# Performance work log

Measured on AMD Instinct MI355X. Metric: run time of the kernel, lower is better.

The kernel has to match this reference:

```python
import jax, jax.numpy as jnp
import numpy as np

N_NODES = 100000
N_EDGES = 1600000
DIM = 128
N_GRAPHS = 64
N_LAYERS = 7
LEAKY_SLOPE = 0.01
BN_EPS = 1e-5


def setup_inputs() -> dict:
    key = jax.random.key(0)
    ks = jax.random.split(key, 6)
    x = jax.random.normal(ks[0], (N_NODES, DIM), dtype=jnp.float32)
    edge_index = jax.random.randint(ks[1], (2, N_EDGES), 0, N_NODES, dtype=jnp.int64)
    batch = jnp.sort(jax.random.randint(ks[2], (N_NODES,), 0, N_GRAPHS, dtype=jnp.int64))
    # GCNConv weights (Glorot-ish scale), biases, BatchNorm affine params
    Ws = jax.random.normal(ks[3], (N_LAYERS, DIM, DIM), dtype=jnp.float32) * (1.0 / np.sqrt(DIM))
    bs = jnp.zeros((N_LAYERS, DIM), dtype=jnp.float32)
    gammas = jnp.ones((N_LAYERS, DIM), dtype=jnp.float32)
    betas = jnp.zeros((N_LAYERS, DIM), dtype=jnp.float32)
    return {"x": x, "edge_index": edge_index, "batch": batch,
            "Ws": Ws, "bs": bs, "gammas": gammas, "betas": betas}


def reference(x, edge_index, batch, Ws, bs, gammas, betas):
    N = x.shape[0]
    # Add self-loops once (shared by all 7 GCNConv layers)
    loops = jnp.arange(N, dtype=edge_index.dtype)
    src = jnp.concatenate([edge_index[0], loops])  # [E+N]
    dst = jnp.concatenate([edge_index[1], loops])  # [E+N]
    # Symmetric normalization: deg over destination (incl. self-loops)
    deg = jax.ops.segment_sum(jnp.ones_like(dst, dtype=x.dtype), dst, num_segments=N)
    dinv = jax.lax.rsqrt(jnp.maximum(deg, 1.0))  # deg >= 1 from self-loops
    norm = dinv[src] * dinv[dst]                 # [E+N]

    def block(h, W, b, gamma, beta):
        # GCNConv: linear -> gather -> normalized scatter-add
        h = h @ W + b                                            # [N, D]
        msgs = h[src] * norm[:, None]                            # [E+N, D]
        h = jax.ops.segment_sum(msgs, dst, num_segments=N)       # [N, D]
        # LeakyReLU then BatchNorm (batch statistics over nodes)
        h = jax.nn.leaky_relu(h, negative_slope=LEAKY_SLOPE)
        mu = jnp.mean(h, axis=0)
        var = jnp.mean((h - mu) ** 2, axis=0)
        h = (h - mu) * jax.lax.rsqrt(var + BN_EPS) * gamma + beta
        return h

    h = x
    for i in range(N_LAYERS):
        h = block(h, Ws[i], bs[i], gammas[i], betas[i])

    # global_mean_pool over graph ids
    sums = jax.ops.segment_sum(h, batch, num_segments=N_GRAPHS)          # [G, D]
    cnt = jax.ops.segment_sum(jnp.ones((N,), h.dtype), batch, num_segments=N_GRAPHS)
    return sums / jnp.maximum(cnt, 1.0)[:, None]
```

## Files before the change

### kernel.cpp

```cpp
#include <hip/hip_runtime.h>
#include <hip/hip_fp16.h>

#define DIMM 128
#define LEAKY_S 0.01f
#define EPS_BN 1e-5f

typedef _Float16 half8 __attribute__((ext_vector_type(8)));
typedef float f32x4 __attribute__((ext_vector_type(4)));


__global__ __launch_bounds__(256) void k_deg(const int* __restrict__ dst, int* __restrict__ deg, int E, int N) {
    int i = blockIdx.x * 256 + threadIdx.x;
    if (i < E) {
        int d = dst[i];
        if ((unsigned)d < (unsigned)N) atomicAdd(&deg[d], 1);
    }
}

__global__ __launch_bounds__(256) void k_dinv(const int* __restrict__ deg, float* __restrict__ dinv, int N) {
    int i = blockIdx.x * 256 + threadIdx.x;
    if (i < N) dinv[i] = rsqrtf((float)(deg[i] + 1));
}

__global__ __launch_bounds__(256) void k_scanA(const int* __restrict__ deg, int* __restrict__ bsum, int n) {
    __shared__ int ws[4];
    int tid = threadIdx.x, lane = tid & 63, wid = tid >> 6;
    int base = blockIdx.x * 1024;
    int s = 0;
    #pragma unroll
    for (int j = 0; j < 4; ++j) {
        int i = base + j * 256 + tid;
        if (i < n) s += deg[i];
    }
    #pragma unroll
    for (int off = 32; off > 0; off >>= 1) s += __shfl_down(s, (unsigned)off, 64);
    if (lane == 0) ws[wid] = s;
    __syncthreads();
    if (tid == 0) bsum[blockIdx.x] = ws[0] + ws[1] + ws[2] + ws[3];
}

__global__ __launch_bounds__(64) void k_scanB(const int* __restrict__ bsum, int* __restrict__ bofs,
                                              int* __restrict__ rowptr, int nb, int n) {
    if (threadIdx.x == 0) {
        int run = 0;
        for (int j = 0; j < nb; ++j) { bofs[j] = run; run += bsum[j]; }
        rowptr[n] = run;
    }
}

__global__ __launch_bounds__(1024) void k_scanC(const int* __restrict__ deg, const int* __restrict__ bofs,
                                                int* __restrict__ rowptr, int n) {
    __shared__ int wsum[16];
    int tid = threadIdx.x, lane = tid & 63, wid = tid >> 6;
    int i = blockIdx.x * 1024 + tid;
    int v = (i < n) ? deg[i] : 0;
    int s = v;
    #pragma unroll
    for (int off = 1; off < 64; off <<= 1) {
        int t = __shfl_up(s, (unsigned)off, 64);
        if (lane >= off) s += t;
    }
    if (lane == 63) wsum[wid] = s;
    __syncthreads();
    if (wid == 0 && lane < 16) {
        int ws = wsum[lane];
        #pragma unroll
        for (int off = 1; off < 16; off <<= 1) {
            int t = __shfl_up(ws, (unsigned)off, 64);
            if (lane >= off) ws += t;
        }
        wsum[lane] = ws;
    }
    __syncthreads();
    int woff = wid ? wsum[wid - 1] : 0;
    if (i < n) rowptr[i] = bofs[blockIdx.x] + woff + (s - v);
}

__global__ __launch_bounds__(256) void k_fill(const int* __restrict__ src, const int* __restrict__ dst,
                                              const int* __restrict__ rowptr, int* __restrict__ cursor,
                                              const float* __restrict__ dinv,
                                              int2* __restrict__ csr, int E, int N) {
    int i = blockIdx.x * 256 + threadIdx.x;
    if (i < E) {
        int d = dst[i], s = src[i];
        if ((unsigned)d < (unsigned)N && (unsigned)s < (unsigned)N) {
            int pos = atomicAdd(&cursor[d], 1);
            int idx = rowptr[d] + pos;
            csr[idx] = make_int2(s, __float_as_int(dinv[s] * dinv[d]));
        }
    }
}


__global__ __launch_bounds__(128) void k_wbn(const float* __restrict__ W, const float* __restrict__ bias,
                                             const float* __restrict__ stats, const float* __restrict__ gamma,
                                             const float* __restrict__ beta,
                                             __half* __restrict__ Wt, float* __restrict__ bias2,
                                             int ident, float inv_n) {
    __shared__ float red2[2];
    int n = blockIdx.x;
    int k = threadIdx.x;
    float a = 1.f, b = 0.f;
    if (!ident) {
        float mu  = stats[k] * inv_n;
        float var = stats[128 + k] * inv_n - mu * mu;
        a = gamma[k] * rsqrtf(var + EPS_BN);
        b = beta[k] - mu * a;
    }
    float w = W[k * DIMM + n];
    Wt[n * DIMM + k] = __float2half(a * w);
    float p = b * w;
    #pragma unroll
    for (int off = 32; off > 0; off >>= 1) p += __shfl_down(p, (unsigned)off, 64);
    if ((k & 63) == 0) red2[k >> 6] = p;
    __syncthreads();
    if (k == 0) bias2[n] = bias[n] + red2[0] + red2[1];
}


__global__ __launch_bounds__(256) void k_gemm(const void* __restrict__ A, const __half* __restrict__ Wt,
                                              const float* __restrict__ bias2,
                                              __half* __restrict__ out, int N, int a_half) {
    __shared__ char smem[128 * 256];
    int tid = threadIdx.x;
    int lane = tid & 63, wid = tid >> 6;
    int quad = lane >> 4, lm = lane & 15;
    int row0 = blockIdx.x * 128;

    const float*  Af = (const float*)A;
    const __half* Ah = (const __half*)A;
    #pragma unroll
    for (int it = 0; it < 8; ++it) {
        int i = it * 256 + tid;
        int r = i >> 4, c = i & 15;
        int gr = row0 + r;
        union { _Float16 h[8]; uint4 u; } pk;
        if (gr < N) {
            if (a_half) {
                pk.u = *(const uint4*)(Ah + (size_t)gr * DIMM + c * 8);
            } else {
                float4 f0 = *(const float4*)(Af + (size_t)gr * DIMM + c * 8);
                float4 f1 = *(const float4*)(Af + (size_t)gr * DIMM + c * 8 + 4);
                pk.h[0] = (_Float16)f0.x; pk.h[1] = (_Float16)f0.y;
                pk.h[2] = (_Float16)f0.z; pk.h[3] = (_Float16)f0.w;
                pk.h[4] = (_Float16)f1.x; pk.h[5] = (_Float16)f1.y;
                pk.h[6] = (_Float16)f1.z; pk.h[7] = (_Float16)f1.w;
            }
        } else {
            pk.u = make_uint4(0, 0, 0, 0);
        }
        *(uint4*)(smem + r * 256 + ((c ^ (r & 7)) << 4)) = pk.u;
    }

    f32x4 acc[2][8];
    #pragma unroll
    for (int c = 0; c < 8; ++c) {
        float bc = bias2[c * 16 + lm];
        acc[0][c] = (f32x4){bc, bc, bc, bc};
        acc[1][c] = acc[0][c];
    }
    __syncthreads();

    const _Float16* Wt16 = (const _Float16*)Wt;
    #pragma unroll
    for (int kc = 0; kc < 4; ++kc) {
        int sw = ((kc * 4 + quad) ^ (lm & 7)) << 4;
        half8 a0 = *(const half8*)(smem + (wid * 32 + lm) * 256 + sw);
        half8 a1 = *(const half8*)(smem + (wid * 32 + 16 + lm) * 256 + sw);
        #pragma unroll
        for (int c = 0; c < 8; ++c) {
            half8 b = *(const half8*)(Wt16 + (c * 16 + lm) * DIMM + kc * 32 + quad * 8);
            acc[0][c] = __builtin_amdgcn_mfma_f32_16x16x32_f16(a0, b, acc[0][c], 0, 0, 0);
            acc[1][c] = __builtin_amdgcn_mfma_f32_16x16x32_f16(a1, b, acc[1][c], 0, 0, 0);
        }
    }

    __syncthreads();
    #pragma unroll
    for (int r = 0; r < 2; ++r)
        #pragma unroll
        for (int c = 0; c < 8; ++c)
            #pragma unroll
            for (int i = 0; i < 4; ++i) {
                int rit = wid * 32 + r * 16 + quad * 4 + i;
                int col = c * 16 + lm;
                *(_Float16*)(smem + rit * 256 + col * 2) = (_Float16)acc[r][c][i];
            }
    __syncthreads();
    for (int i = tid; i < 128 * 16; i += 256) {
        int r = i >> 4, seg = i & 15;
        int gr = row0 + r;
        if (gr < N)
            ((uint4*)(out + (size_t)gr * DIMM))[seg] = ((const uint4*)(smem + r * 256))[seg];
    }
}


__global__ __launch_bounds__(256) void k_agg(const __half* __restrict__ t, __half* __restrict__ out,
                                             const int* __restrict__ rowptr, const int2* __restrict__ csr,
                                             const float* __restrict__ dinv,
                                             float* __restrict__ stats, int N, int nwaves) {
    int tid = threadIdx.x;
    int lane = tid & 63, wid = tid >> 6;
    int grp = lane >> 4;
    int l16 = lane & 15;
    int gw = blockIdx.x * 4 + wid;

    float sx[8] = {0.f, 0.f, 0.f, 0.f, 0.f, 0.f, 0.f, 0.f};
    float qx[8] = {0.f, 0.f, 0.f, 0.f, 0.f, 0.f, 0.f, 0.f};

    int node = gw;
    int e0 = 0, e1 = 0;
    float di = 0.f;
    int2 c[8];
    if (node < N) {
        e0 = rowptr[node]; e1 = rowptr[node + 1]; di = dinv[node];
        int last = e1 - 1;
        #pragma unroll
        for (int j = 0; j < 8; ++j) {
            int idx = e0 + 4 * j + grp;
            int idxc = idx < last ? idx : last;
            if (idxc < 0) idxc = 0;
            c[j] = csr[idxc];
            if (idx >= e1) c[j].y = 0;
        }
    }

    while (node < N) {
        int nxt = node + nwaves;
        int ep0 = 0, ep1 = 0;
        float dip = 0.f;
        if (nxt < N) { ep0 = rowptr[nxt]; ep1 = rowptr[nxt + 1]; dip = dinv[nxt]; }

        union { half8 h; __half2 h2[4]; } us;
        us.h = *(const half8*)(t + ((size_t)(unsigned)node << 7) + l16 * 8);

        float v[8] = {0.f, 0.f, 0.f, 0.f, 0.f, 0.f, 0.f, 0.f};

        #pragma unroll
        for (int j = 0; j < 8; ++j) {
            float wgt = __int_as_float(c[j].y);
            union { half8 h; __half2 h2[4]; } g;
            g.h = *(const half8*)(t + ((size_t)(unsigned)c[j].x << 7) + l16 * 8);
            #pragma unroll
            for (int p = 0; p < 4; ++p) {
                float2 f = __half22float2(g.h2[p]);
                v[2 * p]     = fmaf(wgt, f.x, v[2 * p]);
                v[2 * p + 1] = fmaf(wgt, f.y, v[2 * p + 1]);
            }
        }

        int2 cn[8];
        {
            int lastn = ep1 - 1;
            #pragma unroll
            for (int j = 0; j < 8; ++j) {
                int idx = ep0 + 4 * j + grp;
                int idxc = idx < lastn ? idx : lastn;
                if (idxc < 0) idxc = 0;
                cn[j] = csr[idxc];
                if (idx >= ep1) cn[j].y = 0;
            }
        }

        for (int e = e0 + 32; e < e1; e += 32) {
            int2 cx[8];
            int last = e1 - 1;
            #pragma unroll
            for (int j = 0; j < 8; ++j) {
                int idx = e + 4 * j + grp;
                int idxc = idx < last ? idx : last;
                cx[j] = csr[idxc];
                if (idx >= e1) cx[j].y = 0;
            }
            #pragma unroll
            for (int j = 0; j < 8; ++j) {
                float wgt = __int_as_float(cx[j].y);
                union { half8 h; __half2 h2[4]; } g;
                g.h = *(const half8*)(t + ((size_t)(unsigned)cx[j].x << 7) + l16 * 8);
                #pragma unroll
                for (int p = 0; p < 4; ++p) {
                    float2 f = __half22float2(g.h2[p]);
                    v[2 * p]     = fmaf(wgt, f.x, v[2 * p]);
                    v[2 * p + 1] = fmaf(wgt, f.y, v[2 * p + 1]);
                }
            }
        }

        float sn = (grp == 0) ? di * di : 0.f;
        #pragma unroll
        for (int p = 0; p < 4; ++p) {
            float2 f = __half22float2(us.h2[p]);
            v[2 * p]     = fmaf(sn, f.x, v[2 * p]);
            v[2 * p + 1] = fmaf(sn, f.y, v[2 * p + 1]);
        }

        #pragma unroll
        for (int i = 0; i < 8; ++i) {
            v[i] += __shfl_down(v[i], 32, 64);
            v[i] += __shfl_down(v[i], 16, 64);
        }
        if (grp == 0) {
            union { _Float16 h[8]; uint4 u4; } pk;
            #pragma unroll
            for (int i = 0; i < 8; ++i) {
                v[i] = v[i] > 0.f ? v[i] : LEAKY_S * v[i];
                sx[i] += v[i];
                qx[i] += v[i] * v[i];
                pk.h[i] = (_Float16)v[i];
            }
            *(uint4*)(out + ((size_t)(unsigned)node << 7) + l16 * 8) = pk.u4;
        }

        #pragma unroll
        for (int j = 0; j < 8; ++j) c[j] = cn[j];
        node = nxt; e0 = ep0; e1 = ep1; di = dip;
    }

    __shared__ float red[4 * 128];
    if (grp == 0) {
        *(float4*)(red + wid * 128 + l16 * 8)     = make_float4(sx[0], sx[1], sx[2], sx[3]);
        *(float4*)(red + wid * 128 + l16 * 8 + 4) = make_float4(sx[4], sx[5], sx[6], sx[7]);
    }
    __syncthreads();
    if (tid < 128) {
        float s = red[tid] + red[128 + tid] + red[256 + tid] + red[384 + tid];
        atomicAdd(&stats[tid], s);
    }
    __syncthreads();
    if (grp == 0) {
        *(float4*)(red + wid * 128 + l16 * 8)     = make_float4(qx[0], qx[1], qx[2], qx[3]);
        *(float4*)(red + wid * 128 + l16 * 8 + 4) = make_float4(qx[4], qx[5], qx[6], qx[7]);
    }
    __syncthreads();
    if (tid < 128) {
        float s = red[tid] + red[128 + tid] + red[256 + tid] + red[384 + tid];
        atomicAdd(&stats[128 + tid], s);
    }
}


__global__ __launch_bounds__(64) void k_cnt_bs(const int* __restrict__ batch, int* __restrict__ cnt, int N, int G) {
    int g = blockIdx.x * 64 + threadIdx.x;
    if (g >= G) return;
    int lo = 0, hi = N;
    while (lo < hi) { int mid = (lo + hi) >> 1; if (batch[mid] < g) lo = mid + 1; else hi = mid; }
    int lb = lo;
    lo = 0; hi = N;
    while (lo < hi) { int mid = (lo + hi) >> 1; if (batch[mid] <= g) lo = mid + 1; else hi = mid; }
    cnt[g] = lo - lb;
}

__global__ __launch_bounds__(128) void k_pool(const __half* __restrict__ h, const int* __restrict__ batch,
                                              float* __restrict__ pool, int N, int G) {
    const int CHUNK = 128;
    int start = blockIdx.x * CHUNK;
    if (start >= N) return;
    int end = min(start + CHUNK, N);
    int tid = threadIdx.x;
    float acc = 0.f;
    int cur = batch[start];
    for (int n = start; n < end; ++n) {
        int g = batch[n];
        if (g != cur) {
            if ((unsigned)cur < (unsigned)G) atomicAdd(&pool[(size_t)cur * DIMM + tid], acc);
            acc = 0.f; cur = g;
        }
        acc += __half2float(h[(size_t)n * DIMM + tid]);
    }
    if ((unsigned)cur < (unsigned)G) atomicAdd(&pool[(size_t)cur * DIMM + tid], acc);
}

__global__ __launch_bounds__(256) void k_poolfin(const float* __restrict__ pool, const int* __restrict__ cnt,
                                                 const float* __restrict__ stats, const float* __restrict__ gamma,
                                                 const float* __restrict__ beta,
                                                 float* __restrict__ out, int G, float inv_n) {
    int idx = blockIdx.x * 256 + threadIdx.x;
    if (idx < G * DIMM) {
        int g = idx >> 7, c = idx & 127;
        float mu  = stats[c] * inv_n;
        float var = stats[128 + c] * inv_n - mu * mu;
        float a = gamma[c] * rsqrtf(var + EPS_BN);
        float b = beta[c] - mu * a;
        float m = pool[idx] / (float)max(cnt[g], 1);
        out[idx] = a * m + b;
    }
}


extern "C" void kernel_launch(void* const* d_in, const int* in_sizes, int n_in,
                              void* d_out, int out_size, void* d_ws, size_t ws_size,
                              hipStream_t stream) {
    const float* x      = (const float*)d_in[0];
    const int*   ei     = (const int*)d_in[1];
    const int*   batch  = (const int*)d_in[2];
    const float* Ws     = (const float*)d_in[3];
    const float* bs     = (const float*)d_in[4];
    const float* gammas = (const float*)d_in[5];
    const float* betas  = (const float*)d_in[6];
    float* outp = (float*)d_out;

    int N = in_sizes[2];
    int E = in_sizes[1] / 2;
    int L = in_sizes[3] / (DIMM * DIMM);
    int G = out_size / DIMM;

    const int* srcv = ei;
    const int* dstv = ei + E;

    int nb = (N + 1023) / 1024;

    char* w = (char*)d_ws;
    auto alloc = [&](size_t bytes) { char* p = w; w += (bytes + 511) & ~size_t(511); return p; };
    int*    deg    = (int*)   alloc((size_t)N * 4);
    int*    cursor = (int*)   alloc((size_t)N * 4);
    int*    rowptr = (int*)   alloc((size_t)(N + 1) * 4);
    int*    bsum   = (int*)   alloc((size_t)nb * 4);
    int*    bofs   = (int*)   alloc((size_t)nb * 4);
    int2*   csr    = (int2*)  alloc((size_t)E * 8);
    float*  dinv   = (float*) alloc((size_t)N * 4);
    __half* hA     = (__half*)alloc((size_t)N * DIMM * 2);
    __half* hB     = (__half*)alloc((size_t)N * DIMM * 2);
    __half* Wt     = (__half*)alloc((size_t)DIMM * DIMM * 2);
    float*  bias2  = (float*) alloc((size_t)DIMM * 4);
    float*  stats  = (float*) alloc((size_t)L * 256 * 4);
    float*  pool   = (float*) alloc((size_t)G * DIMM * 4);
    int*    cnt    = (int*)   alloc((size_t)G * 4);

    hipMemsetAsync(deg,    0, (size_t)N * 4, stream);
    hipMemsetAsync(cursor, 0, (size_t)N * 4, stream);
    hipMemsetAsync(stats,  0, (size_t)L * 256 * 4, stream);
    hipMemsetAsync(pool,   0, (size_t)G * DIMM * 4, stream);

    float inv_n = 1.0f / (float)N;

    k_deg  <<<(E + 255) / 256, 256, 0, stream>>>(dstv, deg, E, N);
    k_dinv <<<(N + 255) / 256, 256, 0, stream>>>(deg, dinv, N);
    k_scanA<<<nb, 256, 0, stream>>>(deg, bsum, N);
    k_scanB<<<1, 64, 0, stream>>>(bsum, bofs, rowptr, nb, N);
    k_scanC<<<nb, 1024, 0, stream>>>(deg, bofs, rowptr, N);
    k_fill <<<(E + 255) / 256, 256, 0, stream>>>(srcv, dstv, rowptr, cursor, dinv, csr, E, N);

    const void* cur_in = (const void*)x;
    int a_half = 0;
    for (int l = 0; l < L; ++l) {
        const float* st = (l > 0) ? stats + (size_t)(l - 1) * 256 : stats;
        const float* gm = (l > 0) ? gammas + (size_t)(l - 1) * DIMM : gammas;
        const float* bt = (l > 0) ? betas + (size_t)(l - 1) * DIMM : betas;
        k_wbn<<<DIMM, DIMM, 0, stream>>>(Ws + (size_t)l * DIMM * DIMM, bs + (size_t)l * DIMM,
                                         st, gm, bt, Wt, bias2, (l == 0) ? 1 : 0, inv_n);
        k_gemm<<<(N + 127) / 128, 256, 0, stream>>>(cur_in, Wt, bias2, hA, N, a_half);
        const int nblk = 2048;
        k_agg<<<nblk, 256, 0, stream>>>(hA, hB, rowptr, csr, dinv,
                                        stats + (size_t)l * 256, N, nblk * 4);
        cur_in = (const void*)hB;
        a_half = 1;
    }

    k_cnt_bs<<<(G + 63) / 64, 64, 0, stream>>>(batch, cnt, N, G);
    k_pool<<<(N + 127) / 128, 128, 0, stream>>>(hB, batch, pool, N, G);
    k_poolfin<<<(G * DIMM + 255) / 256, 256, 0, stream>>>(pool, cnt, stats + (size_t)(L - 1) * 256,
                                                          gammas + (size_t)(L - 1) * DIMM,
                                                          betas + (size_t)(L - 1) * DIMM, outp, G, inv_n);
}
```

Before: 1.085 ms.

## Deepen software pipeline in aggregation: prefetch next node's gathered rows and two-ahead CSR

Restructures the per-wave node loop in the aggregation kernel into a deeper software pipeline. The feature rows for the next node's first 32 neighbours and its self row are gathered one iteration early, and the CSR entries and rowptr for the node two ahead are loaded one iteration early. The aim is to hide gather latency behind the current node's reduction and store. The cost is higher register pressure from the extra half8 buffers and CSR arrays, which may reduce occupancy.

```diff
diff --git a/kernel.cpp b/kernel.cpp
--- a/kernel.cpp
+++ b/kernel.cpp
@@ -209,10 +209,15 @@
     float sx[8] = {0.f, 0.f, 0.f, 0.f, 0.f, 0.f, 0.f, 0.f};
     float qx[8] = {0.f, 0.f, 0.f, 0.f, 0.f, 0.f, 0.f, 0.f};
 
+    union H8 { half8 h; __half2 h2[4]; };
+
     int node = gw;
-    int e0 = 0, e1 = 0;
-    float di = 0.f;
-    int2 c[8];
+    int e0 = 0, e1 = 0;   float di = 0.f;
+    int ep0 = 0, ep1 = 0; float dip = 0.f;
+    int2 c0[8], c1[8];
+    H8 gd[8]; H8 us;
+    int nxt = node + nwaves;
+
     if (node < N) {
         e0 = rowptr[node]; e1 = rowptr[node + 1]; di = dinv[node];
         int last = e1 - 1;
@@ -221,48 +226,43 @@
             int idx = e0 + 4 * j + grp;
             int idxc = idx < last ? idx : last;
             if (idxc < 0) idxc = 0;
-            c[j] = csr[idxc];
-            if (idx >= e1) c[j].y = 0;
+            c0[j] = csr[idxc];
+            if (idx >= e1) c0[j].y = 0;
+        }
+        #pragma unroll
+        for (int j = 0; j < 8; ++j)
+            gd[j].h = *(const half8*)(t + ((size_t)(unsigned)c0[j].x << 7) + l16 * 8);
+        us.h = *(const half8*)(t + ((size_t)(unsigned)node << 7) + l16 * 8);
+        if (nxt < N) { ep0 = rowptr[nxt]; ep1 = rowptr[nxt + 1]; dip = dinv[nxt]; }
+        int lastn = ep1 - 1;
+        #pragma unroll
+        for (int j = 0; j < 8; ++j) {
+            int idx = ep0 + 4 * j + grp;
+            int idxc = idx < lastn ? idx : lastn;
+            if (idxc < 0) idxc = 0;
+            c1[j] = csr[idxc];
+            if (idx >= ep1) c1[j].y = 0;
         }
     }
 
     while (node < N) {
-        int nxt = node + nwaves;
-        int ep0 = 0, ep1 = 0;
-        float dip = 0.f;
-        if (nxt < N) { ep0 = rowptr[nxt]; ep1 = rowptr[nxt + 1]; dip = dinv[nxt]; }
-
-        union { half8 h; __half2 h2[4]; } us;
-        us.h = *(const half8*)(t + ((size_t)(unsigned)node << 7) + l16 * 8);
+        int n2 = nxt + nwaves;
+        int n2c = n2 < N ? n2 : 0;
+        int f0 = rowptr[n2c], f1 = rowptr[n2c + 1];
+        float di2 = dinv[n2c];
+        if (n2 >= N) { f0 = 0; f1 = 0; di2 = 0.f; }
 
         float v[8] = {0.f, 0.f, 0.f, 0.f, 0.f, 0.f, 0.f, 0.f};
-
         #pragma unroll
         for (int j = 0; j < 8; ++j) {
-            float wgt = __int_as_float(c[j].y);
-            union { half8 h; __half2 h2[4]; } g;
-            g.h = *(const half8*)(t + ((size_t)(unsigned)c[j].x << 7) + l16 * 8);
+            float wgt = __int_as_float(c0[j].y);
             #pragma unroll
             for (int p = 0; p < 4; ++p) {
-                float2 f = __half22float2(g.h2[p]);
+                float2 f = __half22float2(gd[j].h2[p]);
                 v[2 * p]     = fmaf(wgt, f.x, v[2 * p]);
                 v[2 * p + 1] = fmaf(wgt, f.y, v[2 * p + 1]);
             }
         }
-
-        int2 cn[8];
-        {
-            int lastn = ep1 - 1;
-            #pragma unroll
-            for (int j = 0; j < 8; ++j) {
-                int idx = ep0 + 4 * j + grp;
-                int idxc = idx < lastn ? idx : lastn;
-                if (idxc < 0) idxc = 0;
-                cn[j] = csr[idxc];
-                if (idx >= ep1) cn[j].y = 0;
-            }
-        }
-
         for (int e = e0 + 32; e < e1; e += 32) {
             int2 cx[8];
             int last = e1 - 1;
@@ -276,7 +276,7 @@
             #pragma unroll
             for (int j = 0; j < 8; ++j) {
                 float wgt = __int_as_float(cx[j].y);
-                union { half8 h; __half2 h2[4]; } g;
+                H8 g;
                 g.h = *(const half8*)(t + ((size_t)(unsigned)cx[j].x << 7) + l16 * 8);
                 #pragma unroll
                 for (int p = 0; p < 4; ++p) {
@@ -286,13 +286,33 @@
                 }
             }
         }
-
         float sn = (grp == 0) ? di * di : 0.f;
         #pragma unroll
         for (int p = 0; p < 4; ++p) {
             float2 f = __half22float2(us.h2[p]);
             v[2 * p]     = fmaf(sn, f.x, v[2 * p]);
             v[2 * p + 1] = fmaf(sn, f.y, v[2 * p + 1]);
+        }
+
+        #pragma unroll
+        for (int j = 0; j < 8; ++j)
+            gd[j].h = *(const half8*)(t + ((size_t)(unsigned)c1[j].x << 7) + l16 * 8);
+        {
+            int nr = nxt < N ? nxt : 0;
+            us.h = *(const half8*)(t + ((size_t)(unsigned)nr << 7) + l16 * 8);
+        }
+
+        int2 c2[8];
+        {
+            int last2 = f1 - 1;
+            #pragma unroll
+            for (int j = 0; j < 8; ++j) {
+                int idx = f0 + 4 * j + grp;
+                int idxc = idx < last2 ? idx : last2;
+                if (idxc < 0) idxc = 0;
+                c2[j] = csr[idxc];
+                if (idx >= f1) c2[j].y = 0;
+            }
         }
 
         #pragma unroll
@@ -313,8 +333,9 @@
         }
 
         #pragma unroll
-        for (int j = 0; j < 8; ++j) c[j] = cn[j];
+        for (int j = 0; j < 8; ++j) { c0[j] = c1[j]; c1[j] = c2[j]; }
         node = nxt; e0 = ep0; e1 = ep1; di = dip;
+        nxt = n2;  ep0 = f0;  ep1 = f1;  dip = di2;
     }
 
     __shared__ float red[4 * 128];
```

After: 1.092 ms. Within noise of the previous version (+0.6%).
